# Kernel optimization log

Measured on AMD Instinct MI355X. Metric: run time of the kernel, lower is better.

## Reference

```python
import jax, jax.numpy as jnp
import numpy as np

B, I, H = 256, 512, 512


def _lin_init(k, out_dim, in_dim):
    bound = 1.0 / np.sqrt(in_dim)
    kw, kb = jax.random.split(k)
    W = jax.random.uniform(kw, (out_dim, in_dim), minval=-bound, maxval=bound, dtype=jnp.float32)
    b = jax.random.uniform(kb, (out_dim,), minval=-bound, maxval=bound, dtype=jnp.float32)
    return W, b


def setup_inputs() -> dict:
    key = jax.random.key(0)
    ks = jax.random.split(key, 16)
    inp = {}
    inp['inputs'] = jax.random.normal(ks[0], (B, I), dtype=jnp.float32)
    inp['h0'] = jax.random.normal(ks[1], (B, H), dtype=jnp.float32) * 0.1
    inp['c0'] = jax.random.normal(ks[2], (B, H), dtype=jnp.float32) * 0.1
    inp['hebb'] = jax.random.uniform(ks[3], (B, H, H), minval=-0.01, maxval=0.01, dtype=jnp.float32)
    # plastic recurrent weights: w = 0.02*rand - 0.01, alpha = 1e-4*rand
    inp['w'] = 0.02 * jax.random.uniform(ks[4], (H, H), dtype=jnp.float32) - 0.01
    inp['alpha'] = 1e-4 * jax.random.uniform(ks[5], (1, 1, H), dtype=jnp.float32)
    inp['Wxf'], inp['bxf'] = _lin_init(ks[6], H, I)
    inp['Whf'], inp['bhf'] = _lin_init(ks[7], H, H)
    inp['Wxi'], inp['bxi'] = _lin_init(ks[8], H, I)
    inp['Whi'], inp['bhi'] = _lin_init(ks[9], H, H)
    inp['Wxo'], inp['bxo'] = _lin_init(ks[10], H, I)
    inp['Who'], inp['bho'] = _lin_init(ks[11], H, H)
    inp['Wxc'], inp['bxc'] = _lin_init(ks[12], H, I)
    inp['Wmod'], inp['bmod'] = _lin_init(ks[13], 1, H)   # h2mod: H -> 1
    inp['Wfan'], inp['bfan'] = _lin_init(ks[14], H, 1)   # modfanout: 1 -> H
    return inp


def reference(inputs, h0, c0, hebb, w, alpha,
              Wxf, bxf, Whf, bhf, Wxi, bxi, Whi, bhi,
              Wxo, bxo, Who, bho, Wxc, bxc, Wmod, bmod, Wfan, bfan):
    # gates (torch Linear: y = x @ W.T + b)
    fgt = jax.nn.sigmoid(inputs @ Wxf.T + bxf + h0 @ Whf.T + bhf)
    ipt = jax.nn.sigmoid(inputs @ Wxi.T + bxi + h0 @ Whi.T + bhi)
    opt = jax.nn.sigmoid(inputs @ Wxo.T + bxo + h0 @ Who.T + bho)
    # plastic recurrent path: h0 @ (w + alpha * hebb), per-sample fast weights
    h2c = jnp.einsum('bh,bhk->bk', h0, w + alpha * hebb)
    inputstocell = jnp.tanh(inputs @ Wxc.T + bxc + h2c)
    cell = fgt * c0 + ipt * inputstocell
    hactiv = opt * jnp.tanh(cell)
    # Hebbian outer-product trace update with neuromodulated learning rate
    deltahebb = jnp.einsum('bh,bk->bhk', h0, inputstocell)  # [B,H,H]
    myeta = jnp.tanh(hactiv @ Wmod.T + bmod)                # [B,1]
    myeta = myeta * Wfan[:, 0][None, :] + bfan              # modfanout(1->H): [B,H]
    hebb_new = jnp.clip(hebb + myeta[:, None, :] * deltahebb, -2.0, 2.0)
    return hactiv, cell, hebb_new
```

## Files before the change

kernel.cpp:

```cpp
#include <hip/hip_runtime.h>
#include <hip/hip_bf16.h>
#include <math.h>

#define B_ 256
#define I_ 512
#define H_ 512
#define BH (B_*H_)
#define KA 1024

typedef float f4v  __attribute__((ext_vector_type(4)));
typedef short s8v  __attribute__((ext_vector_type(8)));
typedef float f32x4 __attribute__((ext_vector_type(4)));


#define A_ELEMS (256*1024)
#define B_ELEMS (2048*1024)

__global__ __launch_bounds__(256) void k_convert(
    const float* __restrict__ inputs, const float* __restrict__ h0,
    const float* __restrict__ Wxf, const float* __restrict__ Whf,
    const float* __restrict__ Wxi, const float* __restrict__ Whi,
    const float* __restrict__ Wxo, const float* __restrict__ Who,
    const float* __restrict__ Wxc, const float* __restrict__ w,
    ushort* __restrict__ Ahi, ushort* __restrict__ Alo,
    ushort* __restrict__ Bhi, ushort* __restrict__ Blo) {
    const int NTOT = A_ELEMS + B_ELEMS;
    int stride = gridDim.x * blockDim.x;
    for (int f = blockIdx.x * blockDim.x + threadIdx.x; f < NTOT; f += stride) {
        float x; ushort* dhi; ushort* dlo; int idx;
        if (f < A_ELEMS) {
            idx = f;
            int m = f >> 10, k = f & 1023;
            x = (k < 512) ? inputs[m * 512 + k] : h0[m * 512 + (k - 512)];
            dhi = Ahi; dlo = Alo;
        } else {
            idx = f - A_ELEMS;
            int n = idx >> 10, k = idx & 1023;
            int g = n >> 9, ko = n & 511;
            if (k < 512) {
                const float* W = (g == 0) ? Wxf : (g == 1) ? Wxi : (g == 2) ? Wxo : Wxc;
                x = W[ko * 512 + k];
            } else if (g < 3) {
                const float* W = (g == 0) ? Whf : (g == 1) ? Whi : Who;
                x = W[ko * 512 + (k - 512)];
            } else {
                x = w[(size_t)(k - 512) * 512 + ko];
            }
            dhi = Bhi; dlo = Blo;
        }
        __hip_bfloat16 h = __float2bfloat16(x);
        float hf = __bfloat162float(h);
        __hip_bfloat16 l = __float2bfloat16(x - hf);
        dhi[idx] = *(ushort*)&h;
        dlo[idx] = *(ushort*)&l;
    }
}

__global__ __launch_bounds__(256) void k_mfma_gates(
    const ushort* __restrict__ Ahi, const ushort* __restrict__ Alo,
    const ushort* __restrict__ Bhi, const ushort* __restrict__ Blo,
    const float* __restrict__ bxf, const float* __restrict__ bhf,
    const float* __restrict__ bxi, const float* __restrict__ bhi,
    const float* __restrict__ bxo, const float* __restrict__ bho,
    const float* __restrict__ bxc,
    float* __restrict__ pre) {
    int wave = threadIdx.x >> 6, lane = threadIdx.x & 63;
    int tile = blockIdx.x * 4 + wave;
    int m0 = (tile & 15) << 4;
    int n0 = (tile >> 4) << 4;
    int r  = lane & 15;
    int kg = lane >> 4;

    const s8v* pa_hi = (const s8v*)(Ahi + (size_t)(m0 + r) * KA + kg * 8);
    const s8v* pa_lo = (const s8v*)(Alo + (size_t)(m0 + r) * KA + kg * 8);
    const s8v* pb_hi = (const s8v*)(Bhi + (size_t)(n0 + r) * KA + kg * 8);
    const s8v* pb_lo = (const s8v*)(Blo + (size_t)(n0 + r) * KA + kg * 8);

    f32x4 acc = {0.f, 0.f, 0.f, 0.f};
    #pragma unroll 4
    for (int kc = 0; kc < 32; ++kc) {
        s8v ah = pa_hi[kc * 4];
        s8v al = pa_lo[kc * 4];
        s8v bh = pb_hi[kc * 4];
        s8v bl = pb_lo[kc * 4];
        acc = __builtin_amdgcn_mfma_f32_16x16x32_bf16(ah, bh, acc, 0, 0, 0);
        acc = __builtin_amdgcn_mfma_f32_16x16x32_bf16(ah, bl, acc, 0, 0, 0);
        acc = __builtin_amdgcn_mfma_f32_16x16x32_bf16(al, bh, acc, 0, 0, 0);
    }

    int g  = n0 >> 9;
    int ko = (n0 & 511) + r;
    float bias;
    if (g == 0)      bias = bxf[ko] + bhf[ko];
    else if (g == 1) bias = bxi[ko] + bhi[ko];
    else if (g == 2) bias = bxo[ko] + bho[ko];
    else             bias = bxc[ko];
    #pragma unroll
    for (int j = 0; j < 4; ++j) {
        int m = m0 + kg * 4 + j;
        pre[(size_t)g * BH + (size_t)m * H_ + ko] = acc[j] + bias;
    }
}

__global__ __launch_bounds__(512) void k_dotfin(
    const float* __restrict__ hebb, const float* __restrict__ h0,
    const float* __restrict__ pre, const float* __restrict__ c0,
    const float* __restrict__ alpha,
    const float* __restrict__ Wmod, const float* __restrict__ bmod,
    const float* __restrict__ Wfan, const float* __restrict__ bfan,
    float* __restrict__ out, float* __restrict__ v) {

    __shared__ float h0s[H_];
    __shared__ float plds[4 * H_];
    __shared__ float red[8];

    int b = blockIdx.x;
    int t = threadIdx.x;

    h0s[t & 511] = h0[(size_t)b * H_ + (t & 511)];
    __syncthreads();

    int hg = t >> 7;
    int k4 = t & 127;
    const float4* hb4 = (const float4*)hebb + ((size_t)b << 16);
    float4 acc = make_float4(0.f, 0.f, 0.f, 0.f);
    #pragma unroll 8
    for (int r = 0; r < 128; ++r) {
        int h = (hg << 7) + r;
        float s = h0s[h];
        float4 vv = hb4[(size_t)h * 128 + k4];
        acc.x += s * vv.x; acc.y += s * vv.y;
        acc.z += s * vv.z; acc.w += s * vv.w;
    }
    ((float4*)plds)[hg * 128 + k4] = acc;
    __syncthreads();

    int k = t;
    float dot = plds[k] + plds[H_ + k] + plds[2 * H_ + k] + plds[3 * H_ + k];
    size_t off = (size_t)b * H_ + k;
    float pf = pre[0 * BH + off];
    float pi = pre[1 * BH + off];
    float po = pre[2 * BH + off];
    float pc = pre[3 * BH + off];
    float c2 = tanhf(pc + alpha[k] * dot);
    float fg = 1.f / (1.f + expf(-pf));
    float ig = 1.f / (1.f + expf(-pi));
    float og = 1.f / (1.f + expf(-po));
    float cell = fg * c0[off] + ig * c2;
    float ha = og * tanhf(cell);
    out[off] = ha;
    out[BH + off] = cell;

    float x = ha * Wmod[k];
    #pragma unroll
    for (int o = 32; o > 0; o >>= 1) x += __shfl_down(x, o, 64);
    int wid = t >> 6, lane = t & 63;
    if (lane == 0) red[wid] = x;
    __syncthreads();
    float s8 = red[0] + red[1] + red[2] + red[3]
             + red[4] + red[5] + red[6] + red[7];
    float myeta = tanhf(s8 + bmod[0]);
    v[off] = (myeta * Wfan[k] + bfan[k]) * c2;
}

__global__ __launch_bounds__(256) void k_update(
    const float4* __restrict__ hebb, const float* __restrict__ h0,
    const float* __restrict__ v, float* __restrict__ out) {
    const int total = B_ * H_ * (H_ / 4);
    int stride = gridDim.x * blockDim.x;
    int base = blockIdx.x * blockDim.x + threadIdx.x;
    for (int f = total - stride + base; f >= 0; f -= stride) {
        int k4 = f & 127;
        int h  = (f >> 7) & 511;
        int b  = f >> 16;
        float u = h0[(b << 9) + h];
        const float4* vv4 = (const float4*)v;
        float4 vv = vv4[(b << 7) + k4];
        float4 hb = hebb[f];
        f4v r;
        r.x = fminf(fmaxf(hb.x + u * vv.x, -2.f), 2.f);
        r.y = fminf(fmaxf(hb.y + u * vv.y, -2.f), 2.f);
        r.z = fminf(fmaxf(hb.z + u * vv.z, -2.f), 2.f);
        r.w = fminf(fmaxf(hb.w + u * vv.w, -2.f), 2.f);
        __builtin_nontemporal_store(r, (f4v*)(out) + f);
    }
}

extern "C" void kernel_launch(void* const* d_in, const int* in_sizes, int n_in,
                              void* d_out, int out_size, void* d_ws, size_t ws_size,
                              hipStream_t stream) {
    const float* inputs = (const float*)d_in[0];
    const float* h0     = (const float*)d_in[1];
    const float* c0     = (const float*)d_in[2];
    const float* hebb   = (const float*)d_in[3];
    const float* w      = (const float*)d_in[4];
    const float* alpha  = (const float*)d_in[5];
    const float* Wxf = (const float*)d_in[6];  const float* bxf = (const float*)d_in[7];
    const float* Whf = (const float*)d_in[8];  const float* bhf = (const float*)d_in[9];
    const float* Wxi = (const float*)d_in[10]; const float* bxi = (const float*)d_in[11];
    const float* Whi = (const float*)d_in[12]; const float* bhi = (const float*)d_in[13];
    const float* Wxo = (const float*)d_in[14]; const float* bxo = (const float*)d_in[15];
    const float* Who = (const float*)d_in[16]; const float* bho = (const float*)d_in[17];
    const float* Wxc = (const float*)d_in[18]; const float* bxc = (const float*)d_in[19];
    const float* Wmod = (const float*)d_in[20]; const float* bmod = (const float*)d_in[21];
    const float* Wfan = (const float*)d_in[22]; const float* bfan = (const float*)d_in[23];

    float* out = (float*)d_out;
    float* ws  = (float*)d_ws;
    float*  pre  = ws;
    float*  vbuf = ws + 4 * BH;
    ushort* Ahi  = (ushort*)(ws + 5 * BH);
    ushort* Alo  = Ahi + A_ELEMS;
    ushort* Bhi  = Alo + A_ELEMS;
    ushort* Blo  = Bhi + B_ELEMS;

    k_convert<<<2048, 256, 0, stream>>>(inputs, h0,
        Wxf, Whf, Wxi, Whi, Wxo, Who, Wxc, w, Ahi, Alo, Bhi, Blo);
    k_mfma_gates<<<512, 256, 0, stream>>>(Ahi, Alo, Bhi, Blo,
        bxf, bhf, bxi, bhi, bxo, bho, bxc, pre);
    k_dotfin<<<B_, 512, 0, stream>>>(hebb, h0, pre, c0, alpha,
        Wmod, bmod, Wfan, bfan, out, vbuf);
    k_update<<<2048, 256, 0, stream>>>((const float4*)hebb, h0, vbuf,
                                       out + 2 * BH);
}
```

Measured before the change: 189.0 us.

## Split hebb dot product across H chunks into separate kernel with finalize pass

The per-batch hebb·h0 reduction, which streams 256 MB of hebb, is moved out of the fused dotfin kernel into its own kernel. That kernel launches 8 blocks per batch row, each covering 64 rows of H, and writes partial sums to workspace. A separate finalize kernel sums the 8 partials and then computes the gates, cell, hactiv and the modulated v vector. The aim is more parallelism and memory-level concurrency on the large hebb read, since 256 blocks gave too little occupancy. The cost is one extra launch and a partial-sum buffer roundtrip.

```diff
diff --git a/kernel.cpp b/kernel.cpp
--- a/kernel.cpp
+++ b/kernel.cpp
@@ -7,6 +7,8 @@
 #define H_ 512
 #define BH (B_*H_)
 #define KA 1024
+#define NCH 8
+#define HCH (H_/NCH)
 
 typedef float f4v  __attribute__((ext_vector_type(4)));
 typedef short s8v  __attribute__((ext_vector_type(8)));
@@ -102,65 +104,89 @@
     }
 }
 
-__global__ __launch_bounds__(512) void k_dotfin(
+__global__ __launch_bounds__(256) void k_hebbdot(
     const float* __restrict__ hebb, const float* __restrict__ h0,
-    const float* __restrict__ pre, const float* __restrict__ c0,
-    const float* __restrict__ alpha,
+    float* __restrict__ part) {
+    __shared__ float h0s[HCH];
+    __shared__ float4 red[256];
+    int hbid = blockIdx.x;
+    int b  = hbid >> 3;
+    int ch = hbid & 7;
+    int tid = threadIdx.x;
+
+    if (tid < HCH) h0s[tid] = h0[b * H_ + ch * HCH + tid];
+    __syncthreads();
+
+    const float4* hbp = (const float4*)(hebb + ((size_t)b * H_ + (size_t)ch * HCH) * H_);
+    int tk = tid & 127;
+    int th = tid >> 7;
+    float4 acc = make_float4(0.f, 0.f, 0.f, 0.f);
+    #pragma unroll 8
+    for (int r = 0; r < 32; ++r) {
+        int hh = th * 32 + r;
+        float s = h0s[hh];
+        float4 vv = hbp[(size_t)hh * 128 + tk];
+        acc.x += s * vv.x; acc.y += s * vv.y;
+        acc.z += s * vv.z; acc.w += s * vv.w;
+    }
+    red[tid] = acc;
+    __syncthreads();
+    if (tid < 128) {
+        float4 a = red[tid], c = red[tid + 128];
+        float4 o = make_float4(a.x + c.x, a.y + c.y, a.z + c.z, a.w + c.w);
+        ((float4*)(part + ((size_t)ch * B_ + b) * H_))[tid] = o;
+    }
+}
+
+__global__ __launch_bounds__(256) void k_finalize(
+    const float* __restrict__ pre, const float* __restrict__ part,
+    const float* __restrict__ c0, const float* __restrict__ alpha,
     const float* __restrict__ Wmod, const float* __restrict__ bmod,
     const float* __restrict__ Wfan, const float* __restrict__ bfan,
     float* __restrict__ out, float* __restrict__ v) {
 
-    __shared__ float h0s[H_];
-    __shared__ float plds[4 * H_];
-    __shared__ float red[8];
-
     int b = blockIdx.x;
     int t = threadIdx.x;
 
-    h0s[t & 511] = h0[(size_t)b * H_ + (t & 511)];
-    __syncthreads();
-
-    int hg = t >> 7;
-    int k4 = t & 127;
-    const float4* hb4 = (const float4*)hebb + ((size_t)b << 16);
-    float4 acc = make_float4(0.f, 0.f, 0.f, 0.f);
-    #pragma unroll 8
-    for (int r = 0; r < 128; ++r) {
-        int h = (hg << 7) + r;
-        float s = h0s[h];
-        float4 vv = hb4[(size_t)h * 128 + k4];
-        acc.x += s * vv.x; acc.y += s * vv.y;
-        acc.z += s * vv.z; acc.w += s * vv.w;
-    }
-    ((float4*)plds)[hg * 128 + k4] = acc;
-    __syncthreads();
-
-    int k = t;
-    float dot = plds[k] + plds[H_ + k] + plds[2 * H_ + k] + plds[3 * H_ + k];
-    size_t off = (size_t)b * H_ + k;
-    float pf = pre[0 * BH + off];
-    float pi = pre[1 * BH + off];
-    float po = pre[2 * BH + off];
-    float pc = pre[3 * BH + off];
-    float c2 = tanhf(pc + alpha[k] * dot);
-    float fg = 1.f / (1.f + expf(-pf));
-    float ig = 1.f / (1.f + expf(-pi));
-    float og = 1.f / (1.f + expf(-po));
-    float cell = fg * c0[off] + ig * c2;
-    float ha = og * tanhf(cell);
-    out[off] = ha;
-    out[BH + off] = cell;
-
-    float x = ha * Wmod[k];
+    float c2r[2];
+    float local = 0.f;
+    #pragma unroll
+    for (int s = 0; s < 2; ++s) {
+        int k = t + s * 256;
+        float dot = 0.f;
+        #pragma unroll
+        for (int c = 0; c < NCH; ++c) dot += part[((size_t)c * B_ + b) * H_ + k];
+        size_t off = (size_t)b * H_ + k;
+        float pf = pre[0 * BH + off];
+        float pi = pre[1 * BH + off];
+        float po = pre[2 * BH + off];
+        float pc = pre[3 * BH + off];
+        float c2 = tanhf(pc + alpha[k] * dot);
+        float fg = 1.f / (1.f + expf(-pf));
+        float ig = 1.f / (1.f + expf(-pi));
+        float og = 1.f / (1.f + expf(-po));
+        float cell = fg * c0[off] + ig * c2;
+        float ha = og * tanhf(cell);
+        out[off] = ha;
+        out[BH + off] = cell;
+        c2r[s] = c2;
+        local += ha * Wmod[k];
+    }
+    float x = local;
     #pragma unroll
     for (int o = 32; o > 0; o >>= 1) x += __shfl_down(x, o, 64);
+    __shared__ float red[4];
     int wid = t >> 6, lane = t & 63;
     if (lane == 0) red[wid] = x;
     __syncthreads();
-    float s8 = red[0] + red[1] + red[2] + red[3]
-             + red[4] + red[5] + red[6] + red[7];
-    float myeta = tanhf(s8 + bmod[0]);
-    v[off] = (myeta * Wfan[k] + bfan[k]) * c2;
+    float s4 = red[0] + red[1] + red[2] + red[3];
+    float myeta = tanhf(s4 + bmod[0]);
+    #pragma unroll
+    for (int s = 0; s < 2; ++s) {
+        int k = t + s * 256;
+        size_t off = (size_t)b * H_ + k;
+        v[off] = (myeta * Wfan[k] + bfan[k]) * c2r[s];
+    }
 }
 
 __global__ __launch_bounds__(256) void k_update(
@@ -208,8 +234,9 @@
     float* out = (float*)d_out;
     float* ws  = (float*)d_ws;
     float*  pre  = ws;
-    float*  vbuf = ws + 4 * BH;
-    ushort* Ahi  = (ushort*)(ws + 5 * BH);
+    float*  part = ws + 4 * BH;
+    float*  vbuf = ws + 12 * BH;
+    ushort* Ahi  = (ushort*)(ws + 13 * BH);
     ushort* Alo  = Ahi + A_ELEMS;
     ushort* Bhi  = Alo + A_ELEMS;
     ushort* Blo  = Bhi + B_ELEMS;
@@ -218,8 +245,9 @@
         Wxf, Whf, Wxi, Whi, Wxo, Who, Wxc, w, Ahi, Alo, Bhi, Blo);
     k_mfma_gates<<<512, 256, 0, stream>>>(Ahi, Alo, Bhi, Blo,
         bxf, bhf, bxi, bhi, bxo, bho, bxc, pre);
-    k_dotfin<<<B_, 512, 0, stream>>>(hebb, h0, pre, c0, alpha,
-        Wmod, bmod, Wfan, bfan, out, vbuf);
+    k_hebbdot<<<B_ * NCH, 256, 0, stream>>>(hebb, h0, part);
+    k_finalize<<<B_, 256, 0, stream>>>(pre, part, c0, alpha,
+                                       Wmod, bmod, Wfan, bfan, out, vbuf);
     k_update<<<2048, 256, 0, stream>>>((const float4*)hebb, h0, vbuf,
                                        out + 2 * BH);
 }
```

Measured after the change: 188.2 us. About the same (-0.4%).

## Fuse hebb dot and update into one pass with bf16 LDS tile

Applied to the files above, without the earlier changes.

Merges the per-batch dot-product kernel and the Hebbian update kernel into one kernel. Each block handles a 32-column slice of one batch item's hebb matrix. The slice is read from global memory once and kept in LDS as bf16 for the write-back, so the second full read of hebb goes away. The 16 slices of a batch item combine the neuromodulation reduction through global atomics and a spin-wait, which adds a small init kernel. This risks deadlock if the blocks of one batch item are not all resident at once. Storing hebb as bf16 also adds rounding error to hebb_new.

```diff
diff --git a/kernel.cpp b/kernel.cpp
--- a/kernel.cpp
+++ b/kernel.cpp
@@ -7,6 +7,8 @@
 #define H_ 512
 #define BH (B_*H_)
 #define KA 1024
+#define NSL 16
+#define SLC 32
 
 typedef float f4v  __attribute__((ext_vector_type(4)));
 typedef short s8v  __attribute__((ext_vector_type(8)));
@@ -15,6 +17,13 @@
 
 #define A_ELEMS (256*1024)
 #define B_ELEMS (2048*1024)
+
+__global__ __launch_bounds__(256) void k_init(float* __restrict__ eta,
+                                              int* __restrict__ cnt) {
+    int t = threadIdx.x;
+    eta[t] = 0.f;
+    cnt[t] = 0;
+}
 
 __global__ __launch_bounds__(256) void k_convert(
     const float* __restrict__ inputs, const float* __restrict__ h0,
@@ -102,87 +111,111 @@
     }
 }
 
-__global__ __launch_bounds__(512) void k_dotfin(
+__global__ __launch_bounds__(256) void k_fused(
     const float* __restrict__ hebb, const float* __restrict__ h0,
-    const float* __restrict__ pre, const float* __restrict__ c0,
+    const float* __restrict__ pre, const float* __restrict__ c0in,
     const float* __restrict__ alpha,
     const float* __restrict__ Wmod, const float* __restrict__ bmod,
     const float* __restrict__ Wfan, const float* __restrict__ bfan,
-    float* __restrict__ out, float* __restrict__ v) {
-
-    __shared__ float h0s[H_];
-    __shared__ float plds[4 * H_];
-    __shared__ float red[8];
-
-    int b = blockIdx.x;
-    int t = threadIdx.x;
-
-    h0s[t & 511] = h0[(size_t)b * H_ + (t & 511)];
-    __syncthreads();
-
-    int hg = t >> 7;
-    int k4 = t & 127;
-    const float4* hb4 = (const float4*)hebb + ((size_t)b << 16);
-    float4 acc = make_float4(0.f, 0.f, 0.f, 0.f);
-    #pragma unroll 8
-    for (int r = 0; r < 128; ++r) {
-        int h = (hg << 7) + r;
-        float s = h0s[h];
-        float4 vv = hb4[(size_t)h * 128 + k4];
-        acc.x += s * vv.x; acc.y += s * vv.y;
-        acc.z += s * vv.z; acc.w += s * vv.w;
-    }
-    ((float4*)plds)[hg * 128 + k4] = acc;
-    __syncthreads();
-
-    int k = t;
-    float dot = plds[k] + plds[H_ + k] + plds[2 * H_ + k] + plds[3 * H_ + k];
-    size_t off = (size_t)b * H_ + k;
-    float pf = pre[0 * BH + off];
-    float pi = pre[1 * BH + off];
-    float po = pre[2 * BH + off];
-    float pc = pre[3 * BH + off];
-    float c2 = tanhf(pc + alpha[k] * dot);
-    float fg = 1.f / (1.f + expf(-pf));
-    float ig = 1.f / (1.f + expf(-pi));
-    float og = 1.f / (1.f + expf(-po));
-    float cell = fg * c0[off] + ig * c2;
-    float ha = og * tanhf(cell);
-    out[off] = ha;
-    out[BH + off] = cell;
-
-    float x = ha * Wmod[k];
+    float* __restrict__ eta, int* __restrict__ cnt,
+    float* __restrict__ out) {
+
+    __shared__ ushort sh[512][SLC];
+    __shared__ float  h0s[512];
+    __shared__ f4v    red[256];
+    __shared__ float  vsh[SLC] __attribute__((aligned(16)));
+    __shared__ float  myeta_sh;
+
+    int bid = blockIdx.x;
+    int b   = bid >> 4;
+    int sl  = bid & 15;
+    int c0  = sl * SLC;
+    int t   = threadIdx.x;
+
+    h0s[t]       = h0[(size_t)b * H_ + t];
+    h0s[t + 256] = h0[(size_t)b * H_ + t + 256];
+    __syncthreads();
+
+    int r0 = t >> 3;
+    int q  = t & 7;
+    const float* gbase = hebb + ((size_t)b * H_) * H_ + c0 + q * 4;
+
+    f4v acc = {0.f, 0.f, 0.f, 0.f};
     #pragma unroll
-    for (int o = 32; o > 0; o >>= 1) x += __shfl_down(x, o, 64);
-    int wid = t >> 6, lane = t & 63;
-    if (lane == 0) red[wid] = x;
-    __syncthreads();
-    float s8 = red[0] + red[1] + red[2] + red[3]
-             + red[4] + red[5] + red[6] + red[7];
-    float myeta = tanhf(s8 + bmod[0]);
-    v[off] = (myeta * Wfan[k] + bfan[k]) * c2;
-}
-
-__global__ __launch_bounds__(256) void k_update(
-    const float4* __restrict__ hebb, const float* __restrict__ h0,
-    const float* __restrict__ v, float* __restrict__ out) {
-    const int total = B_ * H_ * (H_ / 4);
-    int stride = gridDim.x * blockDim.x;
-    int base = blockIdx.x * blockDim.x + threadIdx.x;
-    for (int f = total - stride + base; f >= 0; f -= stride) {
-        int k4 = f & 127;
-        int h  = (f >> 7) & 511;
-        int b  = f >> 16;
-        float u = h0[(b << 9) + h];
-        const float4* vv4 = (const float4*)v;
-        float4 vv = vv4[(b << 7) + k4];
-        float4 hb = hebb[f];
-        f4v r;
-        r.x = fminf(fmaxf(hb.x + u * vv.x, -2.f), 2.f);
-        r.y = fminf(fmaxf(hb.y + u * vv.y, -2.f), 2.f);
-        r.z = fminf(fmaxf(hb.z + u * vv.z, -2.f), 2.f);
-        r.w = fminf(fmaxf(hb.w + u * vv.w, -2.f), 2.f);
-        __builtin_nontemporal_store(r, (f4v*)(out) + f);
+    for (int s = 0; s < 16; ++s) {
+        int row = r0 + 32 * s;
+        f4v v = __builtin_nontemporal_load((const f4v*)(gbase + (size_t)row * H_));
+        acc += h0s[row] * v;
+        ushort4 u;
+        __hip_bfloat16 b0 = __float2bfloat16(v.x); u.x = *(ushort*)&b0;
+        __hip_bfloat16 b1 = __float2bfloat16(v.y); u.y = *(ushort*)&b1;
+        __hip_bfloat16 b2 = __float2bfloat16(v.z); u.z = *(ushort*)&b2;
+        __hip_bfloat16 b3 = __float2bfloat16(v.w); u.w = *(ushort*)&b3;
+        *(ushort4*)&sh[row][q * 4] = u;
+    }
+    red[t] = acc;
+    __syncthreads();
+    if (t < 128) red[t] += red[t + 128];  __syncthreads();
+    if (t <  64) red[t] += red[t +  64];  __syncthreads();
+    if (t <  32) red[t] += red[t +  32];  __syncthreads();
+    if (t <  16) red[t] += red[t +  16];  __syncthreads();
+    if (t <   8) red[t] += red[t +   8];  __syncthreads();
+
+    int col = c0 + (t & 31);
+    float ep = 0.f, c2v = 0.f;
+    if (t < 32) {
+        float dot = red[t >> 2][t & 3];
+        size_t off = (size_t)b * H_ + col;
+        float pf = pre[0 * BH + off];
+        float pi = pre[1 * BH + off];
+        float po = pre[2 * BH + off];
+        float pc = pre[3 * BH + off];
+        float c2 = tanhf(pc + alpha[col] * dot);
+        float fg = 1.f / (1.f + expf(-pf));
+        float ig = 1.f / (1.f + expf(-pi));
+        float og = 1.f / (1.f + expf(-po));
+        float cell = fg * c0in[off] + ig * c2;
+        float ha = og * tanhf(cell);
+        out[off] = ha;
+        out[BH + off] = cell;
+        c2v = c2;
+        ep = ha * Wmod[col];
+    }
+    if (t < 64) {
+        #pragma unroll
+        for (int o = 32; o > 0; o >>= 1) ep += __shfl_down(ep, o, 64);
+        if (t == 0) {
+            atomicAdd(&eta[b], ep);
+            __hip_atomic_fetch_add(&cnt[b], 1, __ATOMIC_RELEASE,
+                                   __HIP_MEMORY_SCOPE_AGENT);
+            while (__hip_atomic_load(&cnt[b], __ATOMIC_ACQUIRE,
+                                     __HIP_MEMORY_SCOPE_AGENT) < NSL)
+                __builtin_amdgcn_s_sleep(2);
+            float etot = atomicAdd(&eta[b], 0.0f);
+            myeta_sh = tanhf(etot + bmod[0]);
+        }
+    }
+    __syncthreads();
+    if (t < 32) vsh[t & 31] = (myeta_sh * Wfan[col] + bfan[col]) * c2v;
+    __syncthreads();
+
+    f4v vq = *(const f4v*)&vsh[q * 4];
+    float* gout = out + 2 * BH + ((size_t)b * H_) * H_ + c0 + q * 4;
+    #pragma unroll
+    for (int s = 0; s < 16; ++s) {
+        int row = r0 + 32 * s;
+        ushort4 u = *(const ushort4*)&sh[row][q * 4];
+        f4v hb;
+        hb.x = __uint_as_float(((unsigned)u.x) << 16);
+        hb.y = __uint_as_float(((unsigned)u.y) << 16);
+        hb.z = __uint_as_float(((unsigned)u.z) << 16);
+        hb.w = __uint_as_float(((unsigned)u.w) << 16);
+        f4v r = hb + h0s[row] * vq;
+        r.x = fminf(fmaxf(r.x, -2.f), 2.f);
+        r.y = fminf(fmaxf(r.y, -2.f), 2.f);
+        r.z = fminf(fmaxf(r.z, -2.f), 2.f);
+        r.w = fminf(fmaxf(r.w, -2.f), 2.f);
+        __builtin_nontemporal_store(r, (f4v*)(gout + (size_t)row * H_));
     }
 }
 
@@ -208,18 +241,18 @@
     float* out = (float*)d_out;
     float* ws  = (float*)d_ws;
     float*  pre  = ws;
-    float*  vbuf = ws + 4 * BH;
-    ushort* Ahi  = (ushort*)(ws + 5 * BH);
+    float*  eta  = ws + 4 * BH;
+    int*    cnt  = (int*)(ws + 4 * BH + 256);
+    ushort* Ahi  = (ushort*)(ws + 4 * BH + 512);
     ushort* Alo  = Ahi + A_ELEMS;
     ushort* Bhi  = Alo + A_ELEMS;
     ushort* Blo  = Bhi + B_ELEMS;
 
+    k_init<<<1, 256, 0, stream>>>(eta, cnt);
     k_convert<<<2048, 256, 0, stream>>>(inputs, h0,
         Wxf, Whf, Wxi, Whi, Wxo, Who, Wxc, w, Ahi, Alo, Bhi, Blo);
     k_mfma_gates<<<512, 256, 0, stream>>>(Ahi, Alo, Bhi, Blo,
         bxf, bhf, bxi, bhi, bxo, bho, bxc, pre);
-    k_dotfin<<<B_, 512, 0, stream>>>(hebb, h0, pre, c0, alpha,
-        Wmod, bmod, Wfan, bfan, out, vbuf);
-    k_update<<<2048, 256, 0, stream>>>((const float4*)hebb, h0, vbuf,
-                                       out + 2 * BH);
-}
+    k_fused<<<B_ * NSL, 256, 0, stream>>>(hebb, h0, pre, c0, alpha,
+        Wmod, bmod, Wfan, bfan, eta, cnt, out);
+}
```

Result: slower. 474.3 us (+151.0%).
